# Performance work log

Hardware: AMD Instinct MI355X
Metric: run time of the kernel (lower is better)

## Reference

```python
import jax, jax.numpy as jnp
import numpy as np

N = 32768
H = 256

def setup_inputs() -> dict:
    key = jax.random.key(0)
    ks = jax.random.split(key, 8)
    def glorot(k, shape):
        fan_in, fan_out = shape
        s = jnp.sqrt(2.0 / (fan_in + fan_out)).astype(jnp.float32)
        return jax.random.normal(k, shape, dtype=jnp.float32) * s
    inp = {
        "x_norm": jax.random.normal(ks[0], (N, 3), dtype=jnp.float32),
        "nu": jnp.ones((1,), dtype=jnp.float32) * 0.01,
        "x_std": jnp.array([0.5, 0.5, 0.5], dtype=jnp.float32),
        "y_std": jnp.array([1.2, 1.2, 1.2, 0.8], dtype=jnp.float32),
        "W0": glorot(ks[1], (3, H)), "b0": jnp.zeros((H,), jnp.float32),
        "W1": glorot(ks[2], (H, H)), "b1": jnp.zeros((H,), jnp.float32),
        "W2": glorot(ks[3], (H, H)), "b2": jnp.zeros((H,), jnp.float32),
        "W3": glorot(ks[4], (H, H)), "b3": jnp.zeros((H,), jnp.float32),
        "W4": glorot(ks[5], (H, 4)), "b4": jnp.zeros((4,), jnp.float32),
    }
    return inp

def reference(x_norm, nu, x_std, y_std, W0, b0, W1, b1, W2, b2, W3, b3, W4, b4):
    # per-point MLP: R^3 -> R^4  (u, v, w, p)
    def f(x):
        h = jnp.tanh(x @ W0 + b0)
        h = jnp.tanh(h @ W1 + b1)
        h = jnp.tanh(h @ W2 + b2)
        h = jnp.tanh(h @ W3 + b3)
        return h @ W4 + b4  # [4]

    # Fused single-pass derivatives (replaces 13 autograd.grad calls):
    J = jax.vmap(jax.jacfwd(f))(x_norm)                 # [N,4,3] first derivs
    Hfull = jax.vmap(jax.jacfwd(jax.jacfwd(f)))(x_norm) # [N,4,3,3]
    Hdiag = jnp.diagonal(Hfull, axis1=2, axis2=3)       # [N,4,3] d2/dxi2 only

    # de-normalization scaling: y_std[y] / x_std[x]^order
    Js = J * y_std[None, :, None] / x_std[None, None, :]
    Hs = Hdiag * y_std[None, :, None] / (x_std[None, None, :] ** 2)

    continuity = Js[:, 0, 0] + Js[:, 1, 1] + Js[:, 2, 2]  # du/dx+dv/dy+dw/dz
    lap = Hs.sum(-1)                                       # [N,4] laplacians
    nu_s = nu[0]
    momentum_x = Js[:, 3, 0] - nu_s * lap[:, 0]
    momentum_y = Js[:, 3, 1] - nu_s * lap[:, 1]
    momentum_z = Js[:, 3, 2] - nu_s * lap[:, 2]

    phy_loss = continuity ** 2 + momentum_x ** 2 + momentum_y ** 2 + momentum_z ** 2
    return phy_loss  # [N], reduction='none' (already squeezed)
```

## Files before the change

kernel.cpp:

```cpp
#include <hip/hip_runtime.h>
#include <stdint.h>

typedef __attribute__((ext_vector_type(8))) _Float16 half8v;
typedef __attribute__((ext_vector_type(16))) float float16v;
typedef __attribute__((ext_vector_type(4))) float float4v;

#define NPTS_WG 32
#define NCH 5

__device__ __forceinline__ int agp(int c, int g, int p) {
    return ((c * 32 + g) * 32 + p) * 8;
}

__device__ __forceinline__ unsigned short f16b(float x) {
    const _Float16 h = (_Float16)x;
    return __builtin_bit_cast(unsigned short, h);
}

__device__ __forceinline__ uint32_t pk2f16(float a, float b) {
    return (uint32_t)f16b(a) | ((uint32_t)f16b(b) << 16);
}

__device__ __forceinline__ float fast_tanh(float z) {
    const float e = __expf(2.0f * z);
    return 1.0f - 2.0f / (e + 1.0f);
}

__global__ void wt_split_kernel(const float* __restrict__ W1, const float* __restrict__ W2,
                                const float* __restrict__ W3, unsigned short* __restrict__ wt)
{
    const int b = blockIdx.x;
    const int L = b >> 4;
    const int ch = b & 15;
    const int k0 = ch * 16;
    const float* W = (L == 0) ? W1 : (L == 1) ? W2 : W3;
    const int j = threadIdx.x;
    const int wv = j >> 5, l31 = j & 31;
    uint32_t hi[16], lo[16];
#pragma unroll
    for (int e = 0; e < 16; ++e) {
        const float x = W[(k0 + e) * 256 + j];
        const unsigned short h = f16b(x);
        const float hf = (float)__builtin_bit_cast(_Float16, h);
        hi[e] = h;
        lo[e] = f16b(x - hf);
    }
#pragma unroll
    for (int part = 0; part < 2; ++part) {
        const uint32_t* src = part ? lo : hi;
        unsigned short* base = wt +
            ((((size_t)(L * 2 + part) * 8 + wv) * 16 + ch) * 64) * 8;
#pragma unroll
        for (int hh = 0; hh < 2; ++hh) {
            uint4 v;
            const uint32_t* s = src + hh * 8;
            v.x = s[0] | (s[1] << 16);
            v.y = s[2] | (s[3] << 16);
            v.z = s[4] | (s[5] << 16);
            v.w = s[6] | (s[7] << 16);
            *(uint4*)(base + (hh * 32 + l31) * 8) = v;
        }
    }
}

__global__ __launch_bounds__(512, 2)
void pinn_mfma(const float* __restrict__ x_norm, const float* __restrict__ nu,
               const float* __restrict__ x_std, const float* __restrict__ y_std,
               const float* __restrict__ W0, const float* __restrict__ b0,
               const float* __restrict__ b1, const float* __restrict__ b2,
               const float* __restrict__ b3, const float* __restrict__ W4,
               const unsigned short* __restrict__ wt, float* __restrict__ out)
{
    __shared__ unsigned short AH[NCH * 32 * 256];
    __shared__ float w4_lds[256 * 4];
    __shared__ float part_lds[8 * 4 * 32 * 4];
    __shared__ float y_lds[16 * 32];

    const int tid = threadIdx.x;
    const int lane = tid & 63;
    const int wv = tid >> 6;
    const int l31 = lane & 31;
    const int hh = lane >> 5;
    const int base_pt = blockIdx.x * NPTS_WG;

    const float xs0 = x_std[0], xs1 = x_std[1], xs2 = x_std[2];
    const float ixs20 = 1.f / (xs0 * xs0);
    const float ixs21 = 1.f / (xs1 * xs1);
    const float ixs22 = 1.f / (xs2 * xs2);

    if (tid < 256) ((float4*)w4_lds)[tid] = ((const float4*)W4)[tid];

    {
        const int p = tid & 31;
        const int jq = tid >> 5;
        const float x0 = x_norm[(base_pt + p) * 3 + 0];
        const float x1 = x_norm[(base_pt + p) * 3 + 1];
        const float x2 = x_norm[(base_pt + p) * 3 + 2];
#pragma unroll
        for (int hf = 0; hf < 2; ++hf) {
            const int j8 = jq * 16 + hf * 8;
            const int g = 2 * jq + hf;
            float w0r[8], w1r[8], w2r[8], b0r[8];
            *(float4*)&w0r[0] = *(const float4*)&W0[0 * 256 + j8];
            *(float4*)&w0r[4] = *(const float4*)&W0[0 * 256 + j8 + 4];
            *(float4*)&w1r[0] = *(const float4*)&W0[1 * 256 + j8];
            *(float4*)&w1r[4] = *(const float4*)&W0[1 * 256 + j8 + 4];
            *(float4*)&w2r[0] = *(const float4*)&W0[2 * 256 + j8];
            *(float4*)&w2r[4] = *(const float4*)&W0[2 * 256 + j8 + 4];
            *(float4*)&b0r[0] = *(const float4*)&b0[j8];
            *(float4*)&b0r[4] = *(const float4*)&b0[j8 + 4];
            union { unsigned short u[8]; half8v v; } hv[NCH];
#pragma unroll
            for (int e = 0; e < 8; ++e) {
                const float z = b0r[e] + x0 * w0r[e] + x1 * w1r[e] + x2 * w2r[e];
                const float t = fast_tanh(z);
                const float s = 1.f - t * t;
                hv[0].u[e] = f16b(t);
                hv[1].u[e] = f16b(s * w0r[e]);
                hv[2].u[e] = f16b(s * w1r[e]);
                hv[3].u[e] = f16b(s * w2r[e]);
                hv[4].u[e] = f16b(-2.f * t * s *
                    (w0r[e] * w0r[e] * ixs20 + w1r[e] * w1r[e] * ixs21 +
                     w2r[e] * w2r[e] * ixs22));
            }
#pragma unroll
            for (int c = 0; c < NCH; ++c)
                *(half8v*)&AH[agp(c, g, p)] = hv[c].v;
        }
    }
    __syncthreads();

    const float* biases[3] = {b1, b2, b3};
    const int laneq = lane * 8;

    const unsigned short* whb = wt + ((size_t)0 * 8 + wv) * 8192 + laneq;
    const unsigned short* wlb = wt + ((size_t)1 * 8 + wv) * 8192 + laneq;

    half8v wh[3], wl[3], ab[3][NCH];
    wh[0] = *(const half8v*)(whb);
    wl[0] = *(const half8v*)(wlb);
    wh[1] = *(const half8v*)(whb + 512);
    wl[1] = *(const half8v*)(wlb + 512);
#pragma unroll
    for (int c = 0; c < NCH; ++c) {
        ab[0][c] = *(const half8v*)&AH[agp(c, hh, l31)];
        ab[1][c] = *(const half8v*)&AH[agp(c, 2 + hh, l31)];
    }

#pragma unroll 1
    for (int L = 0; L < 3; ++L) {
        const unsigned short* whL = wt + ((size_t)(L * 2 + 0) * 8 + wv) * 8192 + laneq;
        const unsigned short* wlL = wt + ((size_t)(L * 2 + 1) * 8 + wv) * 8192 + laneq;
        float16v acc[NCH];
#pragma unroll
        for (int c = 0; c < NCH; ++c)
#pragma unroll
            for (int e = 0; e < 16; ++e) acc[c][e] = 0.f;

#pragma unroll
        for (int ch = 0; ch < 16; ++ch) {
            if (ch < 14) {
                wh[(ch + 2) % 3] = *(const half8v*)(whL + (ch + 2) * 512);
                wl[(ch + 2) % 3] = *(const half8v*)(wlL + (ch + 2) * 512);
                const int ng = 2 * (ch + 2) + hh;
#pragma unroll
                for (int c = 0; c < NCH; ++c)
                    ab[(ch + 2) % 3][c] = *(const half8v*)&AH[agp(c, ng, l31)];
            }
            __builtin_amdgcn_s_setprio(1);
#pragma unroll
            for (int c = 0; c < NCH; ++c)
                acc[c] = __builtin_amdgcn_mfma_f32_32x32x16_f16(wh[ch % 3], ab[ch % 3][c], acc[c], 0, 0, 0);
#pragma unroll
            for (int c = 0; c < 4; ++c)
                acc[c] = __builtin_amdgcn_mfma_f32_32x32x16_f16(wl[ch % 3], ab[ch % 3][c], acc[c], 0, 0, 0);
            __builtin_amdgcn_s_setprio(0);
        }

        if (L < 2) {
            const unsigned short* whN = wt + ((size_t)((L + 1) * 2 + 0) * 8 + wv) * 8192 + laneq;
            const unsigned short* wlN = wt + ((size_t)((L + 1) * 2 + 1) * 8 + wv) * 8192 + laneq;
            wh[0] = *(const half8v*)(whN);
            wl[0] = *(const half8v*)(wlN);
            wh[1] = *(const half8v*)(whN + 512);
            wl[1] = *(const half8v*)(wlN + 512);
        }

        const float* bL = biases[L];
        __syncthreads();
#pragma unroll
        for (int q = 0; q < 4; ++q) {
            const int j0 = wv * 32 + 8 * q + 4 * hh;
            const int g = wv * 4 + q;
            float bj[4];
            *(float4*)&bj[0] = *(const float4*)&bL[j0];
            float val[NCH][4];
#pragma unroll
            for (int r = 0; r < 4; ++r) {
                const int e = q * 4 + r;
                const float z = acc[0][e] + bj[r];
                const float t = fast_tanh(z);
                const float s = 1.f - t * t;
                const float d1a = acc[1][e], d1b = acc[2][e], d1c = acc[3][e];
                val[0][r] = t;
                val[1][r] = s * d1a;
                val[2][r] = s * d1b;
                val[3][r] = s * d1c;
                val[4][r] = s * acc[4][e] - 2.f * t * s *
                    (d1a * d1a * ixs20 + d1b * d1b * ixs21 + d1c * d1c * ixs22);
            }
#pragma unroll
            for (int c = 0; c < NCH; ++c) {
                const uint32_t u0 = pk2f16(val[c][0], val[c][1]);
                const uint32_t u1 = pk2f16(val[c][2], val[c][3]);
                *(uint2*)&AH[agp(c, g, l31) + 4 * hh] = make_uint2(u0, u1);
            }
        }
        __syncthreads();
        if (L < 2) {
#pragma unroll
            for (int c = 0; c < NCH; ++c) {
                ab[0][c] = *(const half8v*)&AH[agp(c, hh, l31)];
                ab[1][c] = *(const half8v*)&AH[agp(c, 2 + hh, l31)];
            }
        }
    }

    {
        const int l15 = lane & 15;
        const int g4 = lane >> 4;
        const int koct = wv * 32 + 8 * g4;
        const int gr = wv * 4 + g4;
        union { uint32_t u[4]; half8v v; } HB, LB;
#pragma unroll
        for (int i = 0; i < 4; ++i) {
            const float w0v = (l15 < 4) ? w4_lds[(koct + 2 * i) * 4 + l15] : 0.f;
            const float w1v = (l15 < 4) ? w4_lds[(koct + 2 * i + 1) * 4 + l15] : 0.f;
            const unsigned short h0 = f16b(w0v), h1 = f16b(w1v);
            const float r0 = w0v - (float)__builtin_bit_cast(_Float16, h0);
            const float r1 = w1v - (float)__builtin_bit_cast(_Float16, h1);
            HB.u[i] = (uint32_t)h0 | ((uint32_t)h1 << 16);
            LB.u[i] = (uint32_t)f16b(r0) | ((uint32_t)f16b(r1) << 16);
        }
        float4v acc4[4][2];
#pragma unroll
        for (int cc = 0; cc < 4; ++cc)
#pragma unroll
            for (int ph = 0; ph < 2; ++ph) acc4[cc][ph] = (float4v){0.f, 0.f, 0.f, 0.f};
#pragma unroll
        for (int cc = 0; cc < 4; ++cc) {
#pragma unroll
            for (int ph = 0; ph < 2; ++ph) {
                const half8v ah = *(const half8v*)&AH[agp(1 + cc, gr, l15 + 16 * ph)];
                acc4[cc][ph] = __builtin_amdgcn_mfma_f32_16x16x32_f16(HB.v, ah, acc4[cc][ph], 0, 0, 0);
                if (cc < 3)
                    acc4[cc][ph] = __builtin_amdgcn_mfma_f32_16x16x32_f16(LB.v, ah, acc4[cc][ph], 0, 0, 0);
            }
        }
        if (g4 == 0) {
#pragma unroll
            for (int cc = 0; cc < 4; ++cc)
#pragma unroll
                for (int ph = 0; ph < 2; ++ph)
                    *(float4*)&part_lds[((wv * 4 + cc) * 32 + ph * 16 + l15) * 4] =
                        make_float4(acc4[cc][ph][0], acc4[cc][ph][1],
                                    acc4[cc][ph][2], acc4[cc][ph][3]);
        }
    }
    __syncthreads();

    {
        const int p = tid & 31;
        const int co = tid >> 5;
        const int o = co & 3;
        const int c4 = co >> 2;
        float sum = 0.f;
#pragma unroll
        for (int w8 = 0; w8 < 8; ++w8)
            sum += part_lds[((w8 * 4 + c4) * 32 + p) * 4 + o];
        const float scale = (c4 < 3) ? (y_std[o] / x_std[c4]) : y_std[o];
        y_lds[co * 32 + p] = sum * scale;
    }
    __syncthreads();

    if (tid < 32) {
        const int p = tid;
        const float nuv = nu[0];
        #define YV(c4, o) y_lds[(((c4) * 4) + (o)) * 32 + p]
        const float cont = YV(0, 0) + YV(1, 1) + YV(2, 2);
        const float mx = YV(0, 3) - nuv * YV(3, 0);
        const float my = YV(1, 3) - nuv * YV(3, 1);
        const float mz = YV(2, 3) - nuv * YV(3, 2);
        out[base_pt + p] = cont * cont + mx * mx + my * my + mz * mz;
        #undef YV
    }
}

extern "C" void kernel_launch(void* const* d_in, const int* in_sizes, int n_in,
                              void* d_out, int out_size, void* d_ws, size_t ws_size,
                              hipStream_t stream)
{
    const float* x_norm = (const float*)d_in[0];
    const float* nu     = (const float*)d_in[1];
    const float* x_std  = (const float*)d_in[2];
    const float* y_std  = (const float*)d_in[3];
    const float* W0 = (const float*)d_in[4];  const float* b0 = (const float*)d_in[5];
    const float* W1 = (const float*)d_in[6];  const float* b1 = (const float*)d_in[7];
    const float* W2 = (const float*)d_in[8];  const float* b2 = (const float*)d_in[9];
    const float* W3 = (const float*)d_in[10]; const float* b3 = (const float*)d_in[11];
    const float* W4 = (const float*)d_in[12];
    (void)n_in; (void)out_size; (void)ws_size;
    unsigned short* wt = (unsigned short*)d_ws;
    float* out = (float*)d_out;
    const int npts = in_sizes[0] / 3;

    wt_split_kernel<<<48, 256, 0, stream>>>(W1, W2, W3, wt);
    pinn_mfma<<<npts / NPTS_WG, 512, 0, stream>>>(x_norm, nu, x_std, y_std,
        W0, b0, b1, b2, b3, W4, wt, out);
}
```

Measured before the change: 146.4 us.

## Raise occupancy to 4 WGs/CU by aliasing LDS and shrinking prefetch depth

Launch bounds now request 4 workgroups per CU instead of 2. To make that possible, LDS buffers are merged into one aliased region (part_lds and y_lds reuse the activation buffer, w4_lds is dropped in favour of direct global reads of W4). Register pressure is cut by replacing the 3-deep weight/activation prefetch with a 2-slot weight double buffer and loading activation fragments from LDS just in time each step. An extra barrier protects the aliased LDS region. The trade-off is less latency hiding per wave, and likely register spills under the tighter VGPR budget, in exchange for more resident waves.

```diff
diff --git a/kernel.cpp b/kernel.cpp
--- a/kernel.cpp
+++ b/kernel.cpp
@@ -63,7 +63,7 @@
     }
 }
 
-__global__ __launch_bounds__(512, 2)
+__global__ __launch_bounds__(512, 4)
 void pinn_mfma(const float* __restrict__ x_norm, const float* __restrict__ nu,
                const float* __restrict__ x_std, const float* __restrict__ y_std,
                const float* __restrict__ W0, const float* __restrict__ b0,
@@ -71,10 +71,10 @@
                const float* __restrict__ b3, const float* __restrict__ W4,
                const unsigned short* __restrict__ wt, float* __restrict__ out)
 {
-    __shared__ unsigned short AH[NCH * 32 * 256];
-    __shared__ float w4_lds[256 * 4];
-    __shared__ float part_lds[8 * 4 * 32 * 4];
-    __shared__ float y_lds[16 * 32];
+    __shared__ __align__(16) unsigned char smem[NCH * 32 * 256 * 2];
+    unsigned short* AH = (unsigned short*)smem;
+    float* part_lds = (float*)smem;
+    float* y_lds = (float*)(smem + 16384);
 
     const int tid = threadIdx.x;
     const int lane = tid & 63;
@@ -87,8 +87,6 @@
     const float ixs20 = 1.f / (xs0 * xs0);
     const float ixs21 = 1.f / (xs1 * xs1);
     const float ixs22 = 1.f / (xs2 * xs2);
-
-    if (tid < 256) ((float4*)w4_lds)[tid] = ((const float4*)W4)[tid];
 
     {
         const int p = tid & 31;
@@ -133,20 +131,6 @@
     const float* biases[3] = {b1, b2, b3};
     const int laneq = lane * 8;
 
-    const unsigned short* whb = wt + ((size_t)0 * 8 + wv) * 8192 + laneq;
-    const unsigned short* wlb = wt + ((size_t)1 * 8 + wv) * 8192 + laneq;
-
-    half8v wh[3], wl[3], ab[3][NCH];
-    wh[0] = *(const half8v*)(whb);
-    wl[0] = *(const half8v*)(wlb);
-    wh[1] = *(const half8v*)(whb + 512);
-    wl[1] = *(const half8v*)(wlb + 512);
-#pragma unroll
-    for (int c = 0; c < NCH; ++c) {
-        ab[0][c] = *(const half8v*)&AH[agp(c, hh, l31)];
-        ab[1][c] = *(const half8v*)&AH[agp(c, 2 + hh, l31)];
-    }
-
 #pragma unroll 1
     for (int L = 0; L < 3; ++L) {
         const unsigned short* whL = wt + ((size_t)(L * 2 + 0) * 8 + wv) * 8192 + laneq;
@@ -157,33 +141,36 @@
 #pragma unroll
             for (int e = 0; e < 16; ++e) acc[c][e] = 0.f;
 
+        half8v whA = *(const half8v*)(whL);
+        half8v wlA = *(const half8v*)(wlL);
+        half8v whB, wlB;
+
 #pragma unroll
         for (int ch = 0; ch < 16; ++ch) {
-            if (ch < 14) {
-                wh[(ch + 2) % 3] = *(const half8v*)(whL + (ch + 2) * 512);
-                wl[(ch + 2) % 3] = *(const half8v*)(wlL + (ch + 2) * 512);
-                const int ng = 2 * (ch + 2) + hh;
-#pragma unroll
-                for (int c = 0; c < NCH; ++c)
-                    ab[(ch + 2) % 3][c] = *(const half8v*)&AH[agp(c, ng, l31)];
-            }
+            if (ch < 15) {
+                if ((ch & 1) == 0) {
+                    whB = *(const half8v*)(whL + (ch + 1) * 512);
+                    wlB = *(const half8v*)(wlL + (ch + 1) * 512);
+                } else {
+                    whA = *(const half8v*)(whL + (ch + 1) * 512);
+                    wlA = *(const half8v*)(wlL + (ch + 1) * 512);
+                }
+            }
+            half8v a[NCH];
+            const int g = 2 * ch + hh;
+#pragma unroll
+            for (int c = 0; c < NCH; ++c)
+                a[c] = *(const half8v*)&AH[agp(c, g, l31)];
+            const half8v wh = ((ch & 1) == 0) ? whA : whB;
+            const half8v wl = ((ch & 1) == 0) ? wlA : wlB;
             __builtin_amdgcn_s_setprio(1);
 #pragma unroll
             for (int c = 0; c < NCH; ++c)
-                acc[c] = __builtin_amdgcn_mfma_f32_32x32x16_f16(wh[ch % 3], ab[ch % 3][c], acc[c], 0, 0, 0);
+                acc[c] = __builtin_amdgcn_mfma_f32_32x32x16_f16(wh, a[c], acc[c], 0, 0, 0);
 #pragma unroll
             for (int c = 0; c < 4; ++c)
-                acc[c] = __builtin_amdgcn_mfma_f32_32x32x16_f16(wl[ch % 3], ab[ch % 3][c], acc[c], 0, 0, 0);
+                acc[c] = __builtin_amdgcn_mfma_f32_32x32x16_f16(wl, a[c], acc[c], 0, 0, 0);
             __builtin_amdgcn_s_setprio(0);
-        }
-
-        if (L < 2) {
-            const unsigned short* whN = wt + ((size_t)((L + 1) * 2 + 0) * 8 + wv) * 8192 + laneq;
-            const unsigned short* wlN = wt + ((size_t)((L + 1) * 2 + 1) * 8 + wv) * 8192 + laneq;
-            wh[0] = *(const half8v*)(whN);
-            wl[0] = *(const half8v*)(wlN);
-            wh[1] = *(const half8v*)(whN + 512);
-            wl[1] = *(const half8v*)(wlN + 512);
         }
 
         const float* bL = biases[L];
@@ -217,13 +204,6 @@
             }
         }
         __syncthreads();
-        if (L < 2) {
-#pragma unroll
-            for (int c = 0; c < NCH; ++c) {
-                ab[0][c] = *(const half8v*)&AH[agp(c, hh, l31)];
-                ab[1][c] = *(const half8v*)&AH[agp(c, 2 + hh, l31)];
-            }
-        }
     }
 
     {
@@ -234,8 +214,8 @@
         union { uint32_t u[4]; half8v v; } HB, LB;
 #pragma unroll
         for (int i = 0; i < 4; ++i) {
-            const float w0v = (l15 < 4) ? w4_lds[(koct + 2 * i) * 4 + l15] : 0.f;
-            const float w1v = (l15 < 4) ? w4_lds[(koct + 2 * i + 1) * 4 + l15] : 0.f;
+            const float w0v = (l15 < 4) ? W4[(koct + 2 * i) * 4 + l15] : 0.f;
+            const float w1v = (l15 < 4) ? W4[(koct + 2 * i + 1) * 4 + l15] : 0.f;
             const unsigned short h0 = f16b(w0v), h1 = f16b(w1v);
             const float r0 = w0v - (float)__builtin_bit_cast(_Float16, h0);
             const float r1 = w1v - (float)__builtin_bit_cast(_Float16, h1);
@@ -257,6 +237,7 @@
                     acc4[cc][ph] = __builtin_amdgcn_mfma_f32_16x16x32_f16(LB.v, ah, acc4[cc][ph], 0, 0, 0);
             }
         }
+        __syncthreads();
         if (g4 == 0) {
 #pragma unroll
             for (int cc = 0; cc < 4; ++cc)
```

Measured after the change: 145.2 us. About the same (-0.9%).
